# Optimization experiments

Measured on AMD Instinct MI355X. Metric: run time of the kernel, lower is better.

The kernel has to match this reference:

```python
import jax, jax.numpy as jnp
import numpy as np

SEQ_LEN = 16384
IN_DIM = 2048
STATE_DIM = 2048


def setup_inputs() -> dict:
    key = jax.random.key(0)
    k_xs, k_lam, k_win, k_c, k_d = jax.random.split(key, 5)
    xs = jax.random.normal(k_xs, (SEQ_LEN, IN_DIM), dtype=jnp.float32)
    # diagonal state-transition values in (0, 1) for stability
    lam = jax.random.uniform(k_lam, (STATE_DIM,), dtype=jnp.float32)
    w_in = jax.random.normal(k_win, (STATE_DIM, IN_DIM), dtype=jnp.float32) / np.float32(np.sqrt(IN_DIM))
    c_out = jax.random.normal(k_c, (IN_DIM, STATE_DIM), dtype=jnp.float32) / np.float32(np.sqrt(STATE_DIM))
    d_skip = jax.random.normal(k_d, (IN_DIM,), dtype=jnp.float32)
    return {"xs": xs, "lam": lam, "w_in": w_in, "c_out": c_out, "d_skip": d_skip}


def _ssm_cell(a, b):
    # Faithful replication of BaseSSMLayer.ssm_cell (including its use of
    # matrix_pow_i * matrix_pow_i for the first component, exactly as in source).
    matrix_pow_i, bx_i = a
    matrix_pow_j, bx_j = b
    return (matrix_pow_i * matrix_pow_i, matrix_pow_j * bx_i + bx_j)


def reference(xs, lam, w_in, c_out, d_skip):
    seq_len = xs.shape[0]
    # discretize: broadcast diagonal lambda over the sequence -> [L, N]
    lambda_elements = jnp.broadcast_to(lam, (seq_len, lam.shape[0]))
    # preprocess_inputs: vmap(w_in @ x) == xs @ w_in.T  -> [L, N]
    w_in_xs = jnp.einsum('li,ni->ln', xs, w_in)
    _, hs = jax.lax.associative_scan(_ssm_cell, (lambda_elements, w_in_xs))
    # postprocess: y_t = C h_t + D * x_t  -> [L, in_dim]
    return jnp.einsum('ln,on->lo', hs, c_out) + xs * d_skip
```

## Files before the change

### kernel.cpp

```cpp
#include <hip/hip_runtime.h>

#define SEQ   16384
#define DIM   2048
#define CHUNK 128
#define NCHUNK (SEQ / CHUNK)

typedef __attribute__((ext_vector_type(8))) short  short8;
typedef __attribute__((ext_vector_type(4))) short  short4v;
typedef __attribute__((ext_vector_type(4))) float  floatx4;

static __device__ __forceinline__ float bf2f(short s) {
    return __uint_as_float(((unsigned)(unsigned short)s) << 16);
}
static __device__ __forceinline__ short f2bf(float f) {
    unsigned u = __float_as_uint(f);
    u += 0x7fff + ((u >> 16) & 1);
    return (short)(u >> 16);
}

__global__ void cast_kernel(const float* __restrict__ in, short* __restrict__ out, int n4) {
    int i = blockIdx.x * blockDim.x + threadIdx.x;
    if (i >= n4) return;
    float4 v = ((const float4*)in)[i];
    short4v s;
    s.x = f2bf(v.x); s.y = f2bf(v.y); s.z = f2bf(v.z); s.w = f2bf(v.w);
    ((short4v*)out)[i] = s;
}


#define BAR   __builtin_amdgcn_s_barrier()
#define PRIO1 __builtin_amdgcn_s_setprio(1)
#define PRIO0 __builtin_amdgcn_s_setprio(0)
#define LGKM0 asm volatile("s_waitcnt lgkmcnt(0)" ::: "memory")
#define VMC4  asm volatile("s_waitcnt vmcnt(4)" ::: "memory")
#define VMC0  asm volatile("s_waitcnt vmcnt(0)" ::: "memory")

#define STAGE_A(b, h, t) do { \
    const short* _s = Abase + (size_t)(h) * 128 * K + (size_t)(t) * 64; \
    __builtin_amdgcn_global_load_lds(_s + gOff0, &As[b][h][c0 * 8], 16, 0, 0); \
    __builtin_amdgcn_global_load_lds(_s + gOff1, &As[b][h][c1 * 8], 16, 0, 0); \
} while (0)
#define STAGE_B(b, h, t) do { \
    const short* _s = Bbase + (size_t)(h) * 128 * K + (size_t)(t) * 64; \
    __builtin_amdgcn_global_load_lds(_s + gOff0, &Bs[b][h][c0 * 8], 16, 0, 0); \
    __builtin_amdgcn_global_load_lds(_s + gOff1, &Bs[b][h][c1 * 8], 16, 0, 0); \
} while (0)

#define LDA_(dst, b, mh) \
    _Pragma("unroll") \
    for (int mi = 0; mi < 4; mi++) { \
        _Pragma("unroll") \
        for (int ks = 0; ks < 2; ks++) \
            dst[mi][ks] = *(const short8*)&As[b][mh][(arow + mi * 16) * 64 + \
                                                     ((((ks << 2) | quad) ^ sx) << 3)]; \
    }
#define LDB_(dst, b, nh) \
    _Pragma("unroll") \
    for (int ni = 0; ni < 2; ni++) { \
        _Pragma("unroll") \
        for (int ks = 0; ks < 2; ks++) \
            dst[ni][ks] = *(const short8*)&Bs[b][nh][(brow + ni * 16) * 64 + \
                                                     ((((ks << 2) | quad) ^ sx) << 3)]; \
    }
#define MMA(mh, nh, Aset, Bset) \
    _Pragma("unroll") \
    for (int mi = 0; mi < 4; mi++) { \
        _Pragma("unroll") \
        for (int ni = 0; ni < 2; ni++) { \
            acc[mh][nh][mi][ni] = __builtin_amdgcn_mfma_f32_16x16x32_bf16( \
                Aset[mi][0], Bset[ni][0], acc[mh][nh][mi][ni], 0, 0, 0); \
            acc[mh][nh][mi][ni] = __builtin_amdgcn_mfma_f32_16x16x32_bf16( \
                Aset[mi][1], Bset[ni][1], acc[mh][nh][mi][ni], 0, 0, 0); \
        } \
    }

template<int FUSE>
__global__ __launch_bounds__(512, 2)
void gemm_bt(const short* __restrict__ A, const short* __restrict__ B,
             short* __restrict__ Cbf, float* __restrict__ Cf,
             const float* __restrict__ xs, const float* __restrict__ dskip)
{
    constexpr int K  = DIM;
    constexpr int NT = K / 64;

    __shared__ alignas(16) short As[2][2][128 * 64];
    __shared__ alignas(16) short Bs[2][2][128 * 64];

    const int tid = threadIdx.x;
    const int m0  = blockIdx.y * 256;
    const int n0  = blockIdx.x * 256;

    const int lane = tid & 63;
    const int wv   = tid >> 6;
    const int wrow = wv >> 2;
    const int wcol = wv & 3;
    const int l16  = lane & 15;
    const int quad = lane >> 4;
    const int sx   = l16 & 7;
    const int arow = wrow * 64 + l16;
    const int brow = wcol * 32 + l16;

    const int c0 = tid, c1 = tid + 512;
    const int r0 = c0 >> 3, r1 = c1 >> 3;
    const size_t gOff0 = (size_t)r0 * K + (size_t)((((c0 & 7) ^ (r0 & 7))) * 8);
    const size_t gOff1 = (size_t)r1 * K + (size_t)((((c1 & 7) ^ (r1 & 7))) * 8);
    const short* Abase = A + (size_t)m0 * K;
    const short* Bbase = B + (size_t)n0 * K;

    short8  A0[4][2], A1[4][2], B0[2][2], B1[2][2];
    floatx4 acc[2][2][4][2] = {};

    STAGE_A(0, 0, 0); STAGE_B(0, 0, 0); STAGE_A(0, 1, 0); STAGE_B(0, 1, 0);
    STAGE_A(1, 0, 1); STAGE_B(1, 0, 1);
    VMC4;
    BAR;
    LDA_(A0, 0, 0); LDB_(B0, 0, 0);
    STAGE_A(1, 1, 1); STAGE_B(1, 1, 1);

    for (int i = 0; i < NT / 2; ++i) {
        const int tE = (2 * i + 2) & (NT - 1);
        const int tO = (2 * i + 3) & (NT - 1);

        LGKM0;
        STAGE_A(0, 0, tE);
        LDB_(B1, 0, 1); LDA_(A1, 0, 1);
        PRIO1; MMA(0, 0, A0, B0); PRIO0;
        BAR;
        STAGE_B(0, 0, tE);
        PRIO1; MMA(0, 1, A0, B1); PRIO0;
        BAR;
        LGKM0;
        VMC4;
        STAGE_A(0, 1, tE);
        PRIO1; MMA(1, 0, A1, B0); PRIO0;
        LDA_(A0, 1, 0); LDB_(B0, 1, 0);
        BAR;
        STAGE_B(0, 1, tE);
        PRIO1; MMA(1, 1, A1, B1); PRIO0;
        BAR;

        LGKM0;
        STAGE_A(1, 0, tO);
        LDB_(B1, 1, 1); LDA_(A1, 1, 1);
        PRIO1; MMA(0, 0, A0, B0); PRIO0;
        BAR;
        STAGE_B(1, 0, tO);
        PRIO1; MMA(0, 1, A0, B1); PRIO0;
        BAR;
        LGKM0;
        VMC4;
        STAGE_A(1, 1, tO);
        PRIO1; MMA(1, 0, A1, B0); PRIO0;
        LDA_(A0, 0, 0); LDB_(B0, 0, 0);
        BAR;
        STAGE_B(1, 1, tO);
        PRIO1; MMA(1, 1, A1, B1); PRIO0;
        BAR;
    }
    VMC0;

    if (FUSE == 0) {
        #pragma unroll
        for (int mh = 0; mh < 2; mh++)
        #pragma unroll
        for (int mi = 0; mi < 4; mi++) {
            const int rb = m0 + wrow * 64 + mh * 128 + mi * 16 + quad * 4;
            #pragma unroll
            for (int nh = 0; nh < 2; nh++)
            #pragma unroll
            for (int ni = 0; ni < 2; ni++) {
                const int cc = n0 + wcol * 32 + nh * 128 + ni * 16 + l16;
                #pragma unroll
                for (int r = 0; r < 4; r++)
                    Cbf[(size_t)(rb + r) * DIM + cc] = f2bf(acc[mh][nh][mi][ni][r]);
            }
        }
    } else {
        float dsk[2][2];
        #pragma unroll
        for (int nh = 0; nh < 2; nh++)
        #pragma unroll
        for (int ni = 0; ni < 2; ni++)
            dsk[nh][ni] = dskip[n0 + wcol * 32 + nh * 128 + ni * 16 + l16];
        #pragma unroll
        for (int mh = 0; mh < 2; mh++)
        #pragma unroll
        for (int mi = 0; mi < 4; mi++) {
            const int rb = m0 + wrow * 64 + mh * 128 + mi * 16 + quad * 4;
            #pragma unroll
            for (int nh = 0; nh < 2; nh++)
            #pragma unroll
            for (int ni = 0; ni < 2; ni++) {
                const int cc = n0 + wcol * 32 + nh * 128 + ni * 16 + l16;
                #pragma unroll
                for (int r = 0; r < 4; r++) {
                    size_t idx = (size_t)(rb + r) * DIM + cc;
                    Cf[idx] = acc[mh][nh][mi][ni][r] + xs[idx] * dsk[nh][ni];
                }
            }
        }
    }
}

__global__ void scan_pass1(const short* __restrict__ bx, const float* __restrict__ lam,
                           float* __restrict__ blockLast)
{
    int q     = blockIdx.x * 256 + threadIdx.x;
    int n     = q * 4;
    int chunk = blockIdx.y;
    float4 lm = *(const float4*)&lam[n];
    const uint2* p = (const uint2*)(bx + (size_t)chunk * CHUNK * DIM) + q;
    float h0 = 0.f, h1 = 0.f, h2 = 0.f, h3 = 0.f;
    #pragma unroll 16
    for (int i = 0; i < CHUNK; i++) {
        uint2 v = p[(size_t)i * (DIM / 4)];
        h0 = fmaf(lm.x, h0, bf2f((short)(v.x & 0xffffu)));
        h1 = fmaf(lm.y, h1, bf2f((short)(v.x >> 16)));
        h2 = fmaf(lm.z, h2, bf2f((short)(v.y & 0xffffu)));
        h3 = fmaf(lm.w, h3, bf2f((short)(v.y >> 16)));
    }
    float4 o; o.x = h0; o.y = h1; o.z = h2; o.w = h3;
    *(float4*)&blockLast[(size_t)chunk * DIM + n] = o;
}

__global__ void scan_pass2(float* __restrict__ blockLast, const float* __restrict__ lam)
{
    int n = blockIdx.x * 256 + threadIdx.x;
    float lm = lam[n];
    float p = lm;
    #pragma unroll
    for (int i = 0; i < 7; i++) p = p * p;
    float carry = 0.f;
    #pragma unroll 4
    for (int c = 0; c < NCHUNK; c++) {
        float t = blockLast[(size_t)c * DIM + n];
        blockLast[(size_t)c * DIM + n] = carry;
        carry = fmaf(p, carry, t);
    }
}

__global__ void scan_pass3(short* __restrict__ bxh, const float* __restrict__ lam,
                           const float* __restrict__ carry)
{
    int q     = blockIdx.x * 256 + threadIdx.x;
    int n     = q * 4;
    int chunk = blockIdx.y;
    float4 lm = *(const float4*)&lam[n];
    float4 cv = *(const float4*)&carry[(size_t)chunk * DIM + n];
    float h0 = cv.x, h1 = cv.y, h2 = cv.z, h3 = cv.w;
    uint2* p = (uint2*)(bxh + (size_t)chunk * CHUNK * DIM) + q;
    #pragma unroll 16
    for (int i = 0; i < CHUNK; i++) {
        uint2 v = p[(size_t)i * (DIM / 4)];
        h0 = fmaf(lm.x, h0, bf2f((short)(v.x & 0xffffu)));
        h1 = fmaf(lm.y, h1, bf2f((short)(v.x >> 16)));
        h2 = fmaf(lm.z, h2, bf2f((short)(v.y & 0xffffu)));
        h3 = fmaf(lm.w, h3, bf2f((short)(v.y >> 16)));
        uint2 o;
        o.x = (unsigned)(unsigned short)f2bf(h0) | ((unsigned)(unsigned short)f2bf(h1) << 16);
        o.y = (unsigned)(unsigned short)f2bf(h2) | ((unsigned)(unsigned short)f2bf(h3) << 16);
        p[(size_t)i * (DIM / 4)] = o;
    }
}

extern "C" void kernel_launch(void* const* d_in, const int* in_sizes, int n_in,
                              void* d_out, int out_size, void* d_ws, size_t ws_size,
                              hipStream_t stream)
{
    const float* xs    = (const float*)d_in[0];
    const float* lam   = (const float*)d_in[1];
    const float* w_in  = (const float*)d_in[2];
    const float* c_out = (const float*)d_in[3];
    const float* dskip = (const float*)d_in[4];
    float* out = (float*)d_out;

    char*  ws    = (char*)d_ws;
    short* bxh   = (short*)ws;
    short* w_bf  = (short*)(ws + (size_t)64 * 1024 * 1024);
    short* c_bf  = (short*)(ws + (size_t)72 * 1024 * 1024);
    short* xs_bf = (short*)d_out;
    float* blkl  = (float*)((char*)d_out + (size_t)100 * 1024 * 1024);

    cast_kernel<<<SEQ * DIM / 4 / 256, 256, 0, stream>>>(xs, xs_bf, SEQ * DIM / 4);
    cast_kernel<<<DIM * DIM / 4 / 256, 256, 0, stream>>>(w_in, w_bf, DIM * DIM / 4);
    cast_kernel<<<DIM * DIM / 4 / 256, 256, 0, stream>>>(c_out, c_bf, DIM * DIM / 4);

    dim3 ggrid(DIM / 256, SEQ / 256);
    gemm_bt<0><<<ggrid, 512, 0, stream>>>(xs_bf, w_bf, bxh, nullptr, nullptr, nullptr);

    dim3 sgrid(DIM / 1024, NCHUNK);
    scan_pass1<<<sgrid, 256, 0, stream>>>(bxh, lam, blkl);
    scan_pass2<<<DIM / 256, 256, 0, stream>>>(blkl, lam);
    scan_pass3<<<sgrid, 256, 0, stream>>>(bxh, lam, blkl);

    gemm_bt<1><<<ggrid, 512, 0, stream>>>(bxh, c_bf, nullptr, out, xs, dskip);
}
```

Before: 571.6 us.

## Remap GEMM warp tiles to 128x64 with new LDS pipeline; halve scan chunk

New measurement: 642.7 us. 12.4% more time.

```diff
diff --git a/kernel.cpp b/kernel.cpp
--- a/kernel.cpp
+++ b/kernel.cpp
@@ -2,7 +2,7 @@
 
 #define SEQ   16384
 #define DIM   2048
-#define CHUNK 128
+#define CHUNK 64
 #define NCHUNK (SEQ / CHUNK)
 
 typedef __attribute__((ext_vector_type(8))) short  short8;
@@ -31,7 +31,6 @@
 #define BAR   __builtin_amdgcn_s_barrier()
 #define PRIO1 __builtin_amdgcn_s_setprio(1)
 #define PRIO0 __builtin_amdgcn_s_setprio(0)
-#define LGKM0 asm volatile("s_waitcnt lgkmcnt(0)" ::: "memory")
 #define VMC4  asm volatile("s_waitcnt vmcnt(4)" ::: "memory")
 #define VMC0  asm volatile("s_waitcnt vmcnt(0)" ::: "memory")
 
@@ -46,31 +45,31 @@
     __builtin_amdgcn_global_load_lds(_s + gOff1, &Bs[b][h][c1 * 8], 16, 0, 0); \
 } while (0)
 
-#define LDA_(dst, b, mh) \
+#define READ_A(dst, b, g) \
     _Pragma("unroll") \
-    for (int mi = 0; mi < 4; mi++) { \
+    for (int ml = 0; ml < 2; ml++) { \
         _Pragma("unroll") \
         for (int ks = 0; ks < 2; ks++) \
-            dst[mi][ks] = *(const short8*)&As[b][mh][(arow + mi * 16) * 64 + \
-                                                     ((((ks << 2) | quad) ^ sx) << 3)]; \
-    }
-#define LDB_(dst, b, nh) \
+            dst[ml][ks] = *(const short8*)&As[b][wrow][((g) * 32 + ml * 16 + l16) * 64 + \
+                                                       ((((ks << 2) | quad) ^ sx) << 3)]; \
+    }
+#define READ_B(b) \
     _Pragma("unroll") \
-    for (int ni = 0; ni < 2; ni++) { \
+    for (int ni = 0; ni < 4; ni++) { \
         _Pragma("unroll") \
         for (int ks = 0; ks < 2; ks++) \
-            dst[ni][ks] = *(const short8*)&Bs[b][nh][(brow + ni * 16) * 64 + \
-                                                     ((((ks << 2) | quad) ^ sx) << 3)]; \
-    }
-#define MMA(mh, nh, Aset, Bset) \
+            bR[ni][ks] = *(const short8*)&Bs[b][bhalf][(brow0 + ni * 16) * 64 + \
+                                                       ((((ks << 2) | quad) ^ sx) << 3)]; \
+    }
+#define MMA_G(g, aS) \
     _Pragma("unroll") \
-    for (int mi = 0; mi < 4; mi++) { \
+    for (int ml = 0; ml < 2; ml++) { \
         _Pragma("unroll") \
-        for (int ni = 0; ni < 2; ni++) { \
-            acc[mh][nh][mi][ni] = __builtin_amdgcn_mfma_f32_16x16x32_bf16( \
-                Aset[mi][0], Bset[ni][0], acc[mh][nh][mi][ni], 0, 0, 0); \
-            acc[mh][nh][mi][ni] = __builtin_amdgcn_mfma_f32_16x16x32_bf16( \
-                Aset[mi][1], Bset[ni][1], acc[mh][nh][mi][ni], 0, 0, 0); \
+        for (int ni = 0; ni < 4; ni++) { \
+            acc[(g) * 2 + ml][ni] = __builtin_amdgcn_mfma_f32_16x16x32_bf16( \
+                aS[ml][0], bR[ni][0], acc[(g) * 2 + ml][ni], 0, 0, 0); \
+            acc[(g) * 2 + ml][ni] = __builtin_amdgcn_mfma_f32_16x16x32_bf16( \
+                aS[ml][1], bR[ni][1], acc[(g) * 2 + ml][ni], 0, 0, 0); \
         } \
     }
 
@@ -97,8 +96,8 @@
     const int l16  = lane & 15;
     const int quad = lane >> 4;
     const int sx   = l16 & 7;
-    const int arow = wrow * 64 + l16;
-    const int brow = wcol * 32 + l16;
+    const int bhalf = wcol >> 1;
+    const int brow0 = (wcol & 1) * 64 + l16;
 
     const int c0 = tid, c1 = tid + 512;
     const int r0 = c0 >> 3, r1 = c1 >> 3;
@@ -107,95 +106,77 @@
     const short* Abase = A + (size_t)m0 * K;
     const short* Bbase = B + (size_t)n0 * K;
 
-    short8  A0[4][2], A1[4][2], B0[2][2], B1[2][2];
-    floatx4 acc[2][2][4][2] = {};
-
-    STAGE_A(0, 0, 0); STAGE_B(0, 0, 0); STAGE_A(0, 1, 0); STAGE_B(0, 1, 0);
-    STAGE_A(1, 0, 1); STAGE_B(1, 0, 1);
+    short8  bR[4][2], aE[2][2], aO[2][2];
+    floatx4 acc[8][4] = {};
+
+    STAGE_A(0, 0, 0); STAGE_A(0, 1, 0); STAGE_B(0, 0, 0); STAGE_B(0, 1, 0);
+    STAGE_B(1, 0, 1); STAGE_B(1, 1, 1);
     VMC4;
     BAR;
-    LDA_(A0, 0, 0); LDB_(B0, 0, 0);
-    STAGE_A(1, 1, 1); STAGE_B(1, 1, 1);
-
+
+    #pragma unroll 1
     for (int i = 0; i < NT / 2; ++i) {
-        const int tE = (2 * i + 2) & (NT - 1);
-        const int tO = (2 * i + 3) & (NT - 1);
-
-        LGKM0;
-        STAGE_A(0, 0, tE);
-        LDB_(B1, 0, 1); LDA_(A1, 0, 1);
-        PRIO1; MMA(0, 0, A0, B0); PRIO0;
-        BAR;
-        STAGE_B(0, 0, tE);
-        PRIO1; MMA(0, 1, A0, B1); PRIO0;
-        BAR;
-        LGKM0;
+        const int t1 = 2 * i + 1;
+        const int t2 = (2 * i + 2) & (NT - 1);
+        const int t3 = (2 * i + 3) & (NT - 1);
+
+        READ_B(0); READ_A(aE, 0, 0); READ_A(aO, 0, 1);
+        STAGE_A(1, 0, t1); STAGE_A(1, 1, t1);
+        PRIO1; MMA_G(0, aE); PRIO0;
+        BAR;
+        READ_A(aE, 0, 2); STAGE_B(0, 0, t2);
+        PRIO1; MMA_G(1, aO); PRIO0;
+        BAR;
+        READ_A(aO, 0, 3); STAGE_B(0, 1, t2);
+        PRIO1; MMA_G(2, aE); PRIO0;
+        BAR;
+        PRIO1; MMA_G(3, aO); PRIO0;
         VMC4;
-        STAGE_A(0, 1, tE);
-        PRIO1; MMA(1, 0, A1, B0); PRIO0;
-        LDA_(A0, 1, 0); LDB_(B0, 1, 0);
-        BAR;
-        STAGE_B(0, 1, tE);
-        PRIO1; MMA(1, 1, A1, B1); PRIO0;
-        BAR;
-
-        LGKM0;
-        STAGE_A(1, 0, tO);
-        LDB_(B1, 1, 1); LDA_(A1, 1, 1);
-        PRIO1; MMA(0, 0, A0, B0); PRIO0;
-        BAR;
-        STAGE_B(1, 0, tO);
-        PRIO1; MMA(0, 1, A0, B1); PRIO0;
-        BAR;
-        LGKM0;
+        BAR;
+
+        READ_B(1); READ_A(aE, 1, 0); READ_A(aO, 1, 1);
+        STAGE_A(0, 0, t2);
+        PRIO1; MMA_G(0, aE); PRIO0;
+        BAR;
+        READ_A(aE, 1, 2); STAGE_A(0, 1, t2);
+        PRIO1; MMA_G(1, aO); PRIO0;
+        BAR;
+        READ_A(aO, 1, 3); STAGE_B(1, 0, t3);
+        PRIO1; MMA_G(2, aE); PRIO0;
+        BAR;
+        STAGE_B(1, 1, t3);
+        PRIO1; MMA_G(3, aO); PRIO0;
         VMC4;
-        STAGE_A(1, 1, tO);
-        PRIO1; MMA(1, 0, A1, B0); PRIO0;
-        LDA_(A0, 0, 0); LDB_(B0, 0, 0);
-        BAR;
-        STAGE_B(1, 1, tO);
-        PRIO1; MMA(1, 1, A1, B1); PRIO0;
         BAR;
     }
     VMC0;
 
     if (FUSE == 0) {
         #pragma unroll
-        for (int mh = 0; mh < 2; mh++)
-        #pragma unroll
-        for (int mi = 0; mi < 4; mi++) {
-            const int rb = m0 + wrow * 64 + mh * 128 + mi * 16 + quad * 4;
+        for (int mi = 0; mi < 8; mi++) {
+            const int rb = m0 + wrow * 128 + mi * 16 + quad * 4;
             #pragma unroll
-            for (int nh = 0; nh < 2; nh++)
-            #pragma unroll
-            for (int ni = 0; ni < 2; ni++) {
-                const int cc = n0 + wcol * 32 + nh * 128 + ni * 16 + l16;
+            for (int ni = 0; ni < 4; ni++) {
+                const int cc = n0 + wcol * 64 + ni * 16 + l16;
                 #pragma unroll
                 for (int r = 0; r < 4; r++)
-                    Cbf[(size_t)(rb + r) * DIM + cc] = f2bf(acc[mh][nh][mi][ni][r]);
+                    Cbf[(size_t)(rb + r) * DIM + cc] = f2bf(acc[mi][ni][r]);
             }
         }
     } else {
-        float dsk[2][2];
+        float dsk[4];
         #pragma unroll
-        for (int nh = 0; nh < 2; nh++)
+        for (int ni = 0; ni < 4; ni++) dsk[ni] = dskip[n0 + wcol * 64 + ni * 16 + l16];
         #pragma unroll
-        for (int ni = 0; ni < 2; ni++)
-            dsk[nh][ni] = dskip[n0 + wcol * 32 + nh * 128 + ni * 16 + l16];
-        #pragma unroll
-        for (int mh = 0; mh < 2; mh++)
-        #pragma unroll
-        for (int mi = 0; mi < 4; mi++) {
-            const int rb = m0 + wrow * 64 + mh * 128 + mi * 16 + quad * 4;
+        for (int mi = 0; mi < 8; mi++) {
+            const int rb = m0 + wrow * 128 + mi * 16 + quad * 4;
             #pragma unroll
-            for (int nh = 0; nh < 2; nh++)
-            #pragma unroll
-            for (int ni = 0; ni < 2; ni++) {
-                const int cc = n0 + wcol * 32 + nh * 128 + ni * 16 + l16;
+            for (int ni = 0; ni < 4; ni++) {
+                const int cc = n0 + wcol * 64 + ni * 16 + l16;
                 #pragma unroll
                 for (int r = 0; r < 4; r++) {
                     size_t idx = (size_t)(rb + r) * DIM + cc;
-                    Cf[idx] = acc[mh][nh][mi][ni][r] + xs[idx] * dsk[nh][ni];
+                    Cf[idx] = acc[mi][ni][r] + xs[idx] * dsk[ni];
                 }
             }
         }
@@ -229,7 +210,7 @@
     float lm = lam[n];
     float p = lm;
     #pragma unroll
-    for (int i = 0; i < 7; i++) p = p * p;
+    for (int i = 0; i < 6; i++) p = p * p;
     float carry = 0.f;
     #pragma unroll 4
     for (int c = 0; c < NCHUNK; c++) {
```
